# Kernel tuning notes

Measured on AMD Instinct MI355X. Metric: run time of the kernel, lower is better.

The kernel has to match this reference:

```python
import jax, jax.numpy as jnp
import numpy as np

B, T, H, NH, DH, R = 2, 2048, 1024, 16, 64, 256
ALPHA = 0.6


def setup_inputs() -> dict:
    key = jax.random.key(0)
    ks = jax.random.split(key, 28)
    f32 = jnp.float32

    def nrm(k, shape, s=0.02):
        return jax.random.normal(k, shape, dtype=f32) * s

    inp = {}
    inp['x'] = jax.random.normal(ks[0], (B, T, H), dtype=f32)
    # additive causal mask [1,1,T,T]: 0 on/below diagonal, -1e9 above
    causal = jnp.tril(jnp.ones((T, T), dtype=bool))
    inp['attention_mask'] = jnp.where(causal, 0.0, -1e9).astype(f32)[None, None]
    # low-rank SVD factors for q,k,v,o: Vh [H,R], S [R] (positive), U [H,R], b [H]
    i = 1
    for name in ('q', 'k', 'v', 'o'):
        inp['Vh_' + name] = nrm(ks[i], (H, R)); i += 1
        inp['S_' + name] = jax.random.uniform(ks[i], (R,), dtype=f32, minval=0.5, maxval=1.5); i += 1
        inp['U_' + name] = nrm(ks[i], (H, R)); i += 1
        inp['b_' + name] = jnp.zeros((H,), dtype=f32); i += 1
    # full-rank weights of the original (fallback) attention: y = x @ W + b (Conv1D style)
    for name in ('q', 'k', 'v', 'o'):
        inp['W_' + name] = nrm(ks[i], (H, H)); i += 1
        inp['bf_' + name] = jnp.zeros((H,), dtype=f32); i += 1
    return inp


def _split_heads(t):
    # [B,T,H] -> [B,nH,T,dH]
    Bs, Ts, _ = t.shape
    return t.reshape(Bs, Ts, NH, DH).transpose(0, 2, 1, 3)


def _attention(Q, K, V, mask):
    q, k, v = _split_heads(Q), _split_heads(K), _split_heads(V)
    scores = jnp.einsum('bhtd,bhsd->bhts', q, k) / (DH ** 0.5)
    scores = scores + mask
    w = jax.nn.softmax(scores, axis=-1)
    ctx = jnp.einsum('bhts,bhsd->bhtd', w, v)
    Bs = ctx.shape[0]
    return ctx.transpose(0, 2, 1, 3).reshape(Bs, -1, NH * DH)


def _lowrank(x, Vh, S, U, b):
    # ((x @ Vh) * S) @ U.T + b
    return ((x @ Vh) * S) @ U.T + b


def reference(x, attention_mask,
              Vh_q, S_q, U_q, b_q, Vh_k, S_k, U_k, b_k,
              Vh_v, S_v, U_v, b_v, Vh_o, S_o, U_o, b_o,
              W_q, bf_q, W_k, bf_k, W_v, bf_v, W_o, bf_o):
    # --- low-rank SVD path ---
    Q = _lowrank(x, Vh_q, S_q, U_q, b_q)
    K = _lowrank(x, Vh_k, S_k, U_k, b_k)
    V = _lowrank(x, Vh_v, S_v, U_v, b_v)
    ctx = _attention(Q, K, V, attention_mask)
    out = _lowrank(ctx, Vh_o, S_o, U_o, b_o)
    # --- fallback: original full-rank attention ---
    Qf = x @ W_q + bf_q
    Kf = x @ W_k + bf_k
    Vf = x @ W_v + bf_v
    ctxf = _attention(Qf, Kf, Vf, attention_mask)
    fallback_out = ctxf @ W_o + bf_o
    return ALPHA * out + (1.0 - ALPHA) * fallback_out
```

## Files before the change

kernel.cpp:

```cpp
#include <hip/hip_runtime.h>
#include <hip/hip_bf16.h>

typedef __bf16 bf16_t;
typedef __bf16 bf16x8 __attribute__((ext_vector_type(8)));
typedef float f32x4 __attribute__((ext_vector_type(4)));
typedef _Float16 f16_t;
typedef _Float16 f16x4 __attribute__((ext_vector_type(4)));

#define DEVI static __device__ __forceinline__

static constexpr int TN   = 2048;
static constexpr int Hn   = 1024;
static constexpr int Rn   = 256;
static constexpr int MTOK = 4096;
static constexpr int NCAT = 6144;

static constexpr float QSCALE = 0.125f;
static constexpr float SOFT_OFF = 0.2959399f;

template <typename T>
DEVI void gload16(const T* g, T* l) {
    __builtin_amdgcn_global_load_lds(
        (const __attribute__((address_space(1))) void*)g,
        (__attribute__((address_space(3))) void*)l, 16, 0, 0);
}

DEVI float loadf(const void* base, int idx, bool bfm) {
    if (bfm) {
        unsigned int u = ((const unsigned short*)base)[idx];
        u <<= 16;
        return __builtin_bit_cast(float, u);
    }
    return ((const float*)base)[idx];
}
DEVI bool detect_bf16(const void* mask) {
    return fabsf(((const float*)mask)[0]) > 1.0f;
}

struct PrepArgs {
    const void *x, *mask;
    const void *Vh[4], *S[4], *U[4];
    const void *bb[4], *bfb[4];
    bf16_t *Xb, *Abuf, *Bbuf;
    float *biascat, *biaso;
};

__global__ void k_prep(PrepArgs a) {
    const bool bfm = detect_bf16(a.mask);
    const int bid = blockIdx.x;
    if (bid < 4096) {
        int i = (bid * 256 + threadIdx.x) * 4;
#pragma unroll
        for (int j = 0; j < 4; ++j) a.Xb[i + j] = (bf16_t)loadf(a.x, i + j, bfm);
    } else if (bid < 8192) {
        int idx = (bid - 4096) * 256 + threadIdx.x;
        int proj = idx >> 18;
        int e = idx & 262143;
        int r = e & 255;
        float s = loadf(a.S[proj], r, bfm);
        if (proj == 0) s *= QSCALE;
        if (proj == 3) s *= 0.6f;
        a.Abuf[idx] = (bf16_t)(loadf(a.U[proj], e, bfm) * s);
        a.Bbuf[idx] = (bf16_t)loadf(a.Vh[proj], e, bfm);
    } else {
        int i = (bid - 8192) * 256 + threadIdx.x;
        if (i < 1024)      a.biascat[i] = QSCALE * loadf(a.bb[0], i, bfm);
        else if (i < 2048) a.biascat[i] = loadf(a.bb[1], i - 1024, bfm);
        else if (i < 3072) a.biascat[i] = loadf(a.bb[2], i - 2048, bfm);
        else if (i < 4096) a.biascat[i] = QSCALE * loadf(a.bfb[0], i - 3072, bfm);
        else if (i < 5120) a.biascat[i] = loadf(a.bfb[1], i - 4096, bfm);
        else if (i < 6144) a.biascat[i] = loadf(a.bfb[2], i - 5120, bfm);
        else {
            int j = i - 6144;
            a.biaso[j] = 0.6f * loadf(a.bb[3], j, bfm) + 0.4f * loadf(a.bfb[3], j, bfm);
        }
    }
}

struct TransP { const void* W[4]; bf16_t* dst[4]; int ldd[4]; float scale[4]; const void* mask; };

__global__ void k_transpose4(TransP tp) {
    const bool bfm = detect_bf16(tp.mask);
    const int z = blockIdx.z;
    const void* W = tp.W[z];
    bf16_t* dst = tp.dst[z];
    const int ldd = tp.ldd[z];
    const float scale = tp.scale[z];
    __shared__ float t[32][33];
    int bx = blockIdx.x * 32, by = blockIdx.y * 32;
    int tx = threadIdx.x, ty = threadIdx.y;
#pragma unroll
    for (int k = 0; k < 32; k += 8)
        t[ty + k][tx] = loadf(W, (by + ty + k) * Hn + bx + tx, bfm);
    __syncthreads();
#pragma unroll
    for (int k = 0; k < 32; k += 8)
        dst[(size_t)(bx + ty + k) * ldd + by + tx] = (bf16_t)(scale * t[tx][ty + k]);
}

template <int MI>
DEVI void gemm_stage(const bf16_t* __restrict__ A, int lda,
                     const bf16_t* __restrict__ B, int ldb,
                     int bm, int bn, int kb, bf16_t* Ad, bf16_t* Bd) {
    const int tid = threadIdx.x;
    constexpr int MT = MI * 32;
#pragma unroll
    for (int u = tid; u < MT * 4; u += 256)
        gload16(&A[(size_t)(bm + (u >> 2)) * lda + kb + (u & 3) * 8], &Ad[u * 8]);
#pragma unroll
    for (int u = tid; u < 512; u += 256)
        gload16(&B[(size_t)(bn + (u >> 2)) * ldb + kb + (u & 3) * 8], &Bd[u * 8]);
}

template <int MI>
DEVI void gemm_core_db(const bf16_t* __restrict__ A, int lda,
                       const bf16_t* __restrict__ B, int ldb, int K,
                       bf16_t* Ab0, bf16_t* Ab1, bf16_t* Bb0, bf16_t* Bb1,
                       int bm, int bn, f32x4 (&acc)[MI][4]) {
    const int lane = threadIdx.x & 63;
    const int w    = threadIdx.x >> 6;
    const int wr   = (w >> 1) * (MI * 16);
    const int wc   = (w & 1) * 64;
    const int fr   = lane & 15;
    const int quad = lane >> 4;

#pragma unroll
    for (int i = 0; i < MI; ++i)
#pragma unroll
        for (int j = 0; j < 4; ++j) acc[i][j] = {0.f, 0.f, 0.f, 0.f};

    gemm_stage<MI>(A, lda, B, ldb, bm, bn, 0, Ab0, Bb0);

    const int nk = K >> 5;
    for (int kb = 0; kb < nk; ++kb) {
        const bf16_t* Ac = (kb & 1) ? Ab1 : Ab0;
        const bf16_t* Bc = (kb & 1) ? Bb1 : Bb0;
        __syncthreads();
        if (kb + 1 < nk)
            gemm_stage<MI>(A, lda, B, ldb, bm, bn, (kb + 1) * 32,
                           (kb & 1) ? Ab0 : Ab1, (kb & 1) ? Bb0 : Bb1);
        bf16x8 af[MI], bfv[4];
#pragma unroll
        for (int i = 0; i < MI; ++i)
            af[i] = *(const bf16x8*)&Ac[(wr + i * 16 + fr) * 32 + quad * 8];
#pragma unroll
        for (int j = 0; j < 4; ++j)
            bfv[j] = *(const bf16x8*)&Bc[(wc + j * 16 + fr) * 32 + quad * 8];
#pragma unroll
        for (int i = 0; i < MI; ++i)
#pragma unroll
            for (int j = 0; j < 4; ++j)
                acc[i][j] = __builtin_amdgcn_mfma_f32_16x16x32_bf16(af[i], bfv[j], acc[i][j], 0, 0, 0);
    }
}

template <int MI, bool OUT_DUAL, bool WRITE_VT, int SWZ>
__global__ __launch_bounds__(256)
void k_gemm(const bf16_t* __restrict__ A, int lda,
            const bf16_t* __restrict__ B, int ldb,
            void* __restrict__ C, int ldc, int K,
            const float* __restrict__ bias, const void* __restrict__ mask,
            f16_t* __restrict__ Vt_g) {
    constexpr int MT = MI * 32;
    struct GB { bf16_t A0[MT * 32]; bf16_t A1[MT * 32]; bf16_t B0[4096]; bf16_t B1[4096]; };
    union SM { GB g; f16_t Ls[WRITE_VT ? 128 * 136 : 8]; };
    __shared__ __align__(16) SM sm;

    int bm, bn;
    if constexpr (SWZ == 1) {
        const int id = blockIdx.x, xcd = id & 7, idx = id >> 3;
        bn = (xcd * 6 + idx % 6) * 128;
        bm = (idx / 6) * MT;
    } else if constexpr (SWZ == 2) {
        const int id = blockIdx.x, xcd = id & 7, idx = id >> 3;
        bm = (xcd * 8 + (idx & 7)) * MT;
        bn = (idx >> 3) * 128;
    } else {
        bm = blockIdx.x * MT;
        bn = blockIdx.y * 128;
    }

    const int tid  = threadIdx.x;
    const int lane = tid & 63;
    const int w    = tid >> 6;
    const int wr   = (w >> 1) * (MI * 16);
    const int wc   = (w & 1) * 64;
    const int fr   = lane & 15;
    const int quad = lane >> 4;

    f32x4 acc[MI][4];
    gemm_core_db<MI>(A, lda, B, ldb, K, sm.g.A0, sm.g.A1, sm.g.B0, sm.g.B1, bm, bn, acc);

    if constexpr (WRITE_VT) {
        const bool isV = (bn >= 2048 && bn < 3072) || (bn >= 5120);
        if (isV) {
            const int pth = (bn >= 5120) ? 1 : 0;
            const int colrel = bn - (pth ? 5120 : 2048);
            const int bb = bm >> 11;
            const int R0 = (pth * 32 + bb * 16 + (colrel >> 6)) * 64;
            const int tloc = bm & 2047;
            __syncthreads();
#pragma unroll
            for (int i = 0; i < MI; ++i) {
                const int t0 = wr + i * 16 + quad * 4;
#pragma unroll
                for (int j = 0; j < 4; ++j) {
                    const int c = wc + j * 16 + fr;
                    const float bv = bias[bn + c];
#pragma unroll
                    for (int r = 0; r < 4; ++r)
                        sm.Ls[c * 136 + t0 + r] = (f16_t)(acc[i][j][r] + bv);
                }
            }
            __syncthreads();
            const int c = tid >> 1, seg = tid & 1;
            f16_t* dst = &Vt_g[(size_t)(R0 + c) * TN + tloc + seg * 64];
            const f16_t* src = &sm.Ls[c * 136 + seg * 64];
#pragma unroll
            for (int e = 0; e < 8; ++e)
                *(uint4*)&dst[e * 8] = *(const uint4*)&src[e * 8];
            return;
        }
    }

    bool bfm = false;
    if constexpr (OUT_DUAL) bfm = detect_bf16(mask);
#pragma unroll
    for (int i = 0; i < MI; ++i) {
        const int row0 = bm + wr + i * 16 + quad * 4;
#pragma unroll
        for (int j = 0; j < 4; ++j) {
            const int col = bn + wc + j * 16 + fr;
            const float bv = bias ? bias[col] : 0.f;
#pragma unroll
            for (int r = 0; r < 4; ++r) {
                float v = acc[i][j][r] + bv;
                size_t ci = (size_t)(row0 + r) * ldc + col;
                if constexpr (OUT_DUAL) {
                    if (bfm) ((unsigned short*)C)[ci] = __builtin_bit_cast(unsigned short, (bf16_t)v);
                    else     ((float*)C)[ci] = v;
                } else {
                    ((bf16_t*)C)[ci] = (bf16_t)v;
                }
            }
        }
    }
}

__global__ __launch_bounds__(256)
void k_gemm_small4(const bf16_t* __restrict__ Abuf, const bf16_t* __restrict__ Bbuf,
                   bf16_t* __restrict__ Wcat, bf16_t* __restrict__ WoT) {
    __shared__ __align__(16) bf16_t A0[64 * 32], A1[64 * 32], B0[4096], B1[4096];
    const int z = blockIdx.z;
    const bf16_t* A = Abuf + (size_t)z * Hn * Rn;
    const bf16_t* B = Bbuf + (size_t)z * Hn * Rn;
    bf16_t* C = (z < 3) ? (Wcat + (size_t)z * Hn * Hn) : WoT;
    const int ldc = (z < 3) ? Hn : 2048;

    const int bm = blockIdx.x * 64, bn = blockIdx.y * 128;
    f32x4 acc[2][4];
    gemm_core_db<2>(A, Rn, B, Rn, Rn, A0, A1, B0, B1, bm, bn, acc);

    const int lane = threadIdx.x & 63;
    const int w    = threadIdx.x >> 6;
    const int wr   = (w >> 1) * 32;
    const int wc   = (w & 1) * 64;
    const int fr   = lane & 15;
    const int quad = lane >> 4;
#pragma unroll
    for (int i = 0; i < 2; ++i)
#pragma unroll
        for (int j = 0; j < 4; ++j)
#pragma unroll
            for (int r = 0; r < 4; ++r)
                C[(size_t)(bm + wr + i * 16 + quad * 4 + r) * ldc + bn + wc + j * 16 + fr]
                    = (bf16_t)acc[i][j][r];
}

__global__ __launch_bounds__(256, 4)
void k_flash6(const bf16_t* __restrict__ Y, const f16_t* __restrict__ Vt_g,
              bf16_t* __restrict__ Ctx) {
    const int id   = blockIdx.x;
    const int inst = id & 63;
    const int qt2  = 15 - (id >> 6);
    const int p = inst >> 5, b = (inst >> 4) & 1, h = inst & 15;

    const int tid  = threadIdx.x;
    const int lane = tid & 63;
    const int w    = tid >> 6;
    const int fr   = lane & 15;
    const int quad = lane >> 4;

    const int rowbase = b * TN;
    const int qbase   = qt2 * 128;
    const int qcol = p * 3072 + h * 64;
    const int kcol = qcol + 1024;
    const int ccol = p * 1024 + h * 64;

    __shared__ __align__(16) bf16_t Kb[2][2][64 * 32];
    __shared__ __align__(16) f16_t  Vb[2][64 * 64];

    const int r64 = tid >> 2;
    const int c8  = (tid & 3) * 8;

    size_t vsrc[2];
#pragma unroll
    for (int t = 0; t < 2; ++t) {
        int pp = w * 128 + t * 64 + lane;
        int d  = pp >> 3;
        vsrc[t] = (size_t)(inst * 64 + d) * TN + ((((pp & 7) - d) & 7) * 8);
    }

    f16x4 ones;
#pragma unroll
    for (int j = 0; j < 4; ++j) ones[j] = (f16_t)1.0f;

    bf16x8 qf[2][2];
#pragma unroll
    for (int s = 0; s < 2; ++s) {
        const size_t qrow = (size_t)(rowbase + qbase + s * 64 + w * 16 + fr) * NCAT + qcol;
        qf[s][0] = *(const bf16x8*)&Y[qrow + quad * 8];
        qf[s][1] = *(const bf16x8*)&Y[qrow + 32 + quad * 8];
    }

    f32x4 o[2][4], lacc[2];
#pragma unroll
    for (int s = 0; s < 2; ++s) {
        lacc[s] = {0.f, 0.f, 0.f, 0.f};
#pragma unroll
        for (int db = 0; db < 4; ++db) o[s][db] = {0.f, 0.f, 0.f, 0.f};
    }

    const int t0 = (quad >> 1) + (fr & 7);
    const int h4 = (quad & 1) * 4;

    const int kmax = 2 * qt2 + 1;

    auto stage = [&](int kt, int bsel) {
        const bf16_t* ksrc = &Y[(size_t)(rowbase + kt * 64 + r64) * NCAT + kcol + c8];
        gload16(ksrc,      &Kb[bsel][0][tid * 8]);
        gload16(ksrc + 32, &Kb[bsel][1][tid * 8]);
#pragma unroll
        for (int t = 0; t < 2; ++t)
            gload16(&Vt_g[vsrc[t] + kt * 64], &Vb[bsel][(w * 128 + t * 64 + lane) * 8]);
    };

    stage(0, 0);

    for (int kt = 0; kt <= kmax; ++kt) {
        const int cur = kt & 1;
        __syncthreads();
        if (kt < kmax) stage(kt + 1, cur ^ 1);

#pragma unroll
        for (int s = 0; s < 2; ++s) {
            const int dk = 2 * qt2 + s;
            if (kt > dk) continue;

            f32x4 sacc[4];
#pragma unroll
            for (int nb = 0; nb < 4; ++nb) {
                bf16x8 kf0 = *(const bf16x8*)&Kb[cur][0][(nb * 16 + fr) * 32 + quad * 8];
                bf16x8 kf1 = *(const bf16x8*)&Kb[cur][1][(nb * 16 + fr) * 32 + quad * 8];
                f32x4 t4 = {0.f, 0.f, 0.f, 0.f};
                t4 = __builtin_amdgcn_mfma_f32_16x16x32_bf16(kf0, qf[s][0], t4, 0, 0, 0);
                t4 = __builtin_amdgcn_mfma_f32_16x16x32_bf16(kf1, qf[s][1], t4, 0, 0, 0);
                sacc[nb] = t4;
            }
            if (kt == dk) {
                const int kl = quad * 4;
                const int ql = w * 16 + fr;
#pragma unroll
                for (int nb = 0; nb < 4; ++nb)
#pragma unroll
                    for (int r = 0; r < 4; ++r)
                        if (nb * 16 + kl + r > ql) sacc[nb][r] = -1e30f;
            }

            f16x4 pf[4];
#pragma unroll
            for (int nb = 0; nb < 4; ++nb)
#pragma unroll
                for (int r = 0; r < 4; ++r)
                    pf[nb][r] = (f16_t)__expf(sacc[nb][r] - SOFT_OFF);

#pragma unroll
            for (int nb = 0; nb < 4; ++nb)
                lacc[s] = __builtin_amdgcn_mfma_f32_16x16x16f16(pf[nb], ones, lacc[s], 0, 0, 0);

#pragma unroll
            for (int db = 0; db < 4; ++db) {
                const int vbase = (db * 16 + fr) * 64 + h4;
#pragma unroll
                for (int nb = 0; nb < 4; ++nb) {
                    f16x4 vf = *(const f16x4*)&Vb[cur][vbase + (((nb * 2 + t0) & 7) * 8)];
                    o[s][db] = __builtin_amdgcn_mfma_f32_16x16x16f16(pf[nb], vf, o[s][db], 0, 0, 0);
                }
            }
        }
    }

#pragma unroll
    for (int s = 0; s < 2; ++s)
#pragma unroll
        for (int r = 0; r < 4; ++r) {
            const float inv = 1.0f / lacc[s][r];
            const size_t trow = (size_t)(rowbase + qbase + s * 64 + w * 16 + quad * 4 + r);
#pragma unroll
            for (int db = 0; db < 4; ++db)
                Ctx[trow * 2048 + ccol + db * 16 + fr] = (bf16_t)(o[s][db][r] * inv);
        }
}

extern "C" void kernel_launch(void* const* d_in, const int* in_sizes, int n_in,
                              void* d_out, int out_size, void* d_ws, size_t ws_size,
                              hipStream_t stream) {
    const void* x    = d_in[0];
    const void* mask = d_in[1];
    const void* Vh[4] = { d_in[2],  d_in[6],  d_in[10], d_in[14] };
    const void* Sp[4] = { d_in[3],  d_in[7],  d_in[11], d_in[15] };
    const void* Up[4] = { d_in[4],  d_in[8],  d_in[12], d_in[16] };
    const void* bb[4] = { d_in[5],  d_in[9],  d_in[13], d_in[17] };
    const void* Wp[4] = { d_in[18], d_in[20], d_in[22], d_in[24] };
    const void* bf[4] = { d_in[19], d_in[21], d_in[23], d_in[25] };

    char* ws = (char*)d_ws;
    size_t off = 0;
    auto alloc = [&](size_t bytes) -> void* {
        void* p = ws + off;
        off = (off + bytes + 255) & ~(size_t)255;
        return p;
    };
    bf16_t* Xb      = (bf16_t*)alloc((size_t)MTOK * Hn * 2);
    bf16_t* Wcat    = (bf16_t*)alloc((size_t)NCAT * Hn * 2);
    bf16_t* Yb      = (bf16_t*)alloc((size_t)MTOK * NCAT * 2);
    bf16_t* Ctx     = (bf16_t*)alloc((size_t)MTOK * 2048 * 2);
    bf16_t* WoT     = (bf16_t*)alloc((size_t)Hn * 2048 * 2);
    f16_t*  Vt_g    = (f16_t*)alloc((size_t)64 * 64 * TN * 2);
    bf16_t* Abuf    = (bf16_t*)alloc((size_t)4 * Hn * Rn * 2);
    bf16_t* Bbuf    = (bf16_t*)alloc((size_t)4 * Hn * Rn * 2);
    float*  biascat = (float*)alloc(NCAT * 4);
    float*  biaso   = (float*)alloc(Hn * 4);

    PrepArgs pa;
    pa.x = x; pa.mask = mask;
    for (int i = 0; i < 4; ++i) {
        pa.Vh[i] = Vh[i]; pa.S[i] = Sp[i]; pa.U[i] = Up[i];
        pa.bb[i] = bb[i]; pa.bfb[i] = bf[i];
    }
    pa.Xb = Xb; pa.Abuf = Abuf; pa.Bbuf = Bbuf; pa.biascat = biascat; pa.biaso = biaso;
    k_prep<<<8220, 256, 0, stream>>>(pa);

    TransP tp;
    for (int i = 0; i < 3; ++i) {
        tp.W[i] = Wp[i]; tp.dst[i] = Wcat + (size_t)(3 * Hn + i * Hn) * Hn;
        tp.ldd[i] = Hn; tp.scale[i] = (i == 0) ? QSCALE : 1.0f;
    }
    tp.W[3] = Wp[3]; tp.dst[3] = WoT + 1024; tp.ldd[3] = 2048; tp.scale[3] = 0.4f;
    tp.mask = mask;
    k_transpose4<<<dim3(32, 32, 4), dim3(32, 8), 0, stream>>>(tp);

    k_gemm_small4<<<dim3(16, 8, 4), 256, 0, stream>>>(Abuf, Bbuf, Wcat, WoT);

    k_gemm<4, false, true, 1><<<1536, 256, 0, stream>>>(
        Xb, Hn, Wcat, Hn, Yb, NCAT, Hn, biascat, nullptr, Vt_g);

    k_flash6<<<1024, 256, 0, stream>>>(Yb, Vt_g, Ctx);

    k_gemm<2, true, false, 2><<<512, 256, 0, stream>>>(
        Ctx, 2048, WoT, 2048, d_out, Hn, 2048, biaso, mask, nullptr);
}
```

Baseline: 325.0 us.

## Split-K the output projection GEMM and fold weight transpose into prep kernel

The final output GEMM (K=2048) is split into two K=1024 halves using larger 128-row tiles, each writing fp32 partials into the reused Yb buffer. A new combine kernel sums the partials, adds the bias and writes the output in the detected dtype. The separate weight-transpose launch is merged into the prep kernel as extra blocks to save a launch. The cost is an extra fp32 round trip of 2x4096x1024 partials plus one more kernel.

```diff
diff --git a/kernel.cpp b/kernel.cpp
--- a/kernel.cpp
+++ b/kernel.cpp
@@ -41,6 +41,8 @@
     const void *x, *mask;
     const void *Vh[4], *S[4], *U[4];
     const void *bb[4], *bfb[4];
+    const void *W[4];
+    bf16_t *Wdst[4]; int Wldd[4]; float Wscale[4];
     bf16_t *Xb, *Abuf, *Bbuf;
     float *biascat, *biaso;
 };
@@ -48,12 +50,14 @@
 __global__ void k_prep(PrepArgs a) {
     const bool bfm = detect_bf16(a.mask);
     const int bid = blockIdx.x;
+    const int tid = threadIdx.x;
+    __shared__ float t[32][33];
     if (bid < 4096) {
-        int i = (bid * 256 + threadIdx.x) * 4;
+        int i = (bid * 256 + tid) * 4;
 #pragma unroll
         for (int j = 0; j < 4; ++j) a.Xb[i + j] = (bf16_t)loadf(a.x, i + j, bfm);
     } else if (bid < 8192) {
-        int idx = (bid - 4096) * 256 + threadIdx.x;
+        int idx = (bid - 4096) * 256 + tid;
         int proj = idx >> 18;
         int e = idx & 262143;
         int r = e & 255;
@@ -62,8 +66,8 @@
         if (proj == 3) s *= 0.6f;
         a.Abuf[idx] = (bf16_t)(loadf(a.U[proj], e, bfm) * s);
         a.Bbuf[idx] = (bf16_t)loadf(a.Vh[proj], e, bfm);
-    } else {
-        int i = (bid - 8192) * 256 + threadIdx.x;
+    } else if (bid < 8220) {
+        int i = (bid - 8192) * 256 + tid;
         if (i < 1024)      a.biascat[i] = QSCALE * loadf(a.bb[0], i, bfm);
         else if (i < 2048) a.biascat[i] = loadf(a.bb[1], i - 1024, bfm);
         else if (i < 3072) a.biascat[i] = loadf(a.bb[2], i - 2048, bfm);
@@ -74,28 +78,24 @@
             int j = i - 6144;
             a.biaso[j] = 0.6f * loadf(a.bb[3], j, bfm) + 0.4f * loadf(a.bfb[3], j, bfm);
         }
-    }
-}
-
-struct TransP { const void* W[4]; bf16_t* dst[4]; int ldd[4]; float scale[4]; const void* mask; };
-
-__global__ void k_transpose4(TransP tp) {
-    const bool bfm = detect_bf16(tp.mask);
-    const int z = blockIdx.z;
-    const void* W = tp.W[z];
-    bf16_t* dst = tp.dst[z];
-    const int ldd = tp.ldd[z];
-    const float scale = tp.scale[z];
-    __shared__ float t[32][33];
-    int bx = blockIdx.x * 32, by = blockIdx.y * 32;
-    int tx = threadIdx.x, ty = threadIdx.y;
-#pragma unroll
-    for (int k = 0; k < 32; k += 8)
-        t[ty + k][tx] = loadf(W, (by + ty + k) * Hn + bx + tx, bfm);
-    __syncthreads();
-#pragma unroll
-    for (int k = 0; k < 32; k += 8)
-        dst[(size_t)(bx + ty + k) * ldd + by + tx] = (bf16_t)(scale * t[tx][ty + k]);
+    } else {
+        const int tb = bid - 8220;
+        const int z = tb >> 10;
+        const int t2 = tb & 1023;
+        const int bx = (t2 & 31) * 32, by = (t2 >> 5) * 32;
+        const int tx = tid & 31, ty = tid >> 5;
+        const void* W = a.W[z];
+        bf16_t* dst = a.Wdst[z];
+        const int ldd = a.Wldd[z];
+        const float scale = a.Wscale[z];
+#pragma unroll
+        for (int k = 0; k < 32; k += 8)
+            t[ty + k][tx] = loadf(W, (by + ty + k) * Hn + bx + tx, bfm);
+        __syncthreads();
+#pragma unroll
+        for (int k = 0; k < 32; k += 8)
+            dst[(size_t)(bx + ty + k) * ldd + by + tx] = (bf16_t)(scale * t[tx][ty + k]);
+    }
 }
 
 template <int MI>
@@ -154,13 +154,12 @@
     }
 }
 
-template <int MI, bool OUT_DUAL, bool WRITE_VT, int SWZ>
+template <int MI, int OMODE, bool WRITE_VT, int SWZ>
 __global__ __launch_bounds__(256)
 void k_gemm(const bf16_t* __restrict__ A, int lda,
             const bf16_t* __restrict__ B, int ldb,
             void* __restrict__ C, int ldc, int K,
-            const float* __restrict__ bias, const void* __restrict__ mask,
-            f16_t* __restrict__ Vt_g) {
+            const float* __restrict__ bias, f16_t* __restrict__ Vt_g) {
     constexpr int MT = MI * 32;
     struct GB { bf16_t A0[MT * 32]; bf16_t A1[MT * 32]; bf16_t B0[4096]; bf16_t B1[4096]; };
     union SM { GB g; f16_t Ls[WRITE_VT ? 128 * 136 : 8]; };
@@ -171,10 +170,15 @@
         const int id = blockIdx.x, xcd = id & 7, idx = id >> 3;
         bn = (xcd * 6 + idx % 6) * 128;
         bm = (idx / 6) * MT;
-    } else if constexpr (SWZ == 2) {
-        const int id = blockIdx.x, xcd = id & 7, idx = id >> 3;
-        bm = (xcd * 8 + (idx & 7)) * MT;
-        bn = (idx >> 3) * 128;
+    } else if constexpr (SWZ == 3) {
+        const int id = blockIdx.x;
+        const int ksel = id >> 8;
+        const int idx  = id & 255;
+        bn = (idx & 7) * 128;
+        bm = (idx >> 3) * MT;
+        A += ksel * 1024;
+        B += ksel * 1024;
+        C = (void*)((float*)C + (size_t)ksel * MTOK * 1024);
     } else {
         bm = blockIdx.x * MT;
         bn = blockIdx.y * 128;
@@ -223,27 +227,36 @@
         }
     }
 
-    bool bfm = false;
-    if constexpr (OUT_DUAL) bfm = detect_bf16(mask);
 #pragma unroll
     for (int i = 0; i < MI; ++i) {
         const int row0 = bm + wr + i * 16 + quad * 4;
 #pragma unroll
         for (int j = 0; j < 4; ++j) {
             const int col = bn + wc + j * 16 + fr;
-            const float bv = bias ? bias[col] : 0.f;
+            const float bv = (OMODE == 0 && bias) ? bias[col] : 0.f;
 #pragma unroll
             for (int r = 0; r < 4; ++r) {
                 float v = acc[i][j][r] + bv;
                 size_t ci = (size_t)(row0 + r) * ldc + col;
-                if constexpr (OUT_DUAL) {
-                    if (bfm) ((unsigned short*)C)[ci] = __builtin_bit_cast(unsigned short, (bf16_t)v);
-                    else     ((float*)C)[ci] = v;
-                } else {
-                    ((bf16_t*)C)[ci] = (bf16_t)v;
-                }
+                if constexpr (OMODE == 2) ((float*)C)[ci] = v;
+                else                      ((bf16_t*)C)[ci] = (bf16_t)v;
             }
         }
+    }
+}
+
+__global__ void k_combine(const float* __restrict__ P, const float* __restrict__ biaso,
+                          void* __restrict__ out, const void* __restrict__ mask) {
+    const bool bfm = detect_bf16(mask);
+    const int i = (blockIdx.x * 256 + threadIdx.x) * 4;
+    const f32x4 p0 = *(const f32x4*)&P[i];
+    const f32x4 p1 = *(const f32x4*)&P[i + MTOK * 1024];
+    const int col = i & 1023;
+#pragma unroll
+    for (int j = 0; j < 4; ++j) {
+        float v = p0[j] + p1[j] + biaso[col + j];
+        if (bfm) ((unsigned short*)out)[i + j] = __builtin_bit_cast(unsigned short, (bf16_t)v);
+        else     ((float*)out)[i + j] = v;
     }
 }
 
@@ -441,32 +454,32 @@
     bf16_t* Bbuf    = (bf16_t*)alloc((size_t)4 * Hn * Rn * 2);
     float*  biascat = (float*)alloc(NCAT * 4);
     float*  biaso   = (float*)alloc(Hn * 4);
+    float*  Psplit  = (float*)Yb;
 
     PrepArgs pa;
     pa.x = x; pa.mask = mask;
     for (int i = 0; i < 4; ++i) {
         pa.Vh[i] = Vh[i]; pa.S[i] = Sp[i]; pa.U[i] = Up[i];
         pa.bb[i] = bb[i]; pa.bfb[i] = bf[i];
-    }
+        pa.W[i] = Wp[i];
+    }
+    for (int i = 0; i < 3; ++i) {
+        pa.Wdst[i] = Wcat + (size_t)(3 * Hn + i * Hn) * Hn;
+        pa.Wldd[i] = Hn; pa.Wscale[i] = (i == 0) ? QSCALE : 1.0f;
+    }
+    pa.Wdst[3] = WoT + 1024; pa.Wldd[3] = 2048; pa.Wscale[3] = 0.4f;
     pa.Xb = Xb; pa.Abuf = Abuf; pa.Bbuf = Bbuf; pa.biascat = biascat; pa.biaso = biaso;
-    k_prep<<<8220, 256, 0, stream>>>(pa);
-
-    TransP tp;
-    for (int i = 0; i < 3; ++i) {
-        tp.W[i] = Wp[i]; tp.dst[i] = Wcat + (size_t)(3 * Hn + i * Hn) * Hn;
-        tp.ldd[i] = Hn; tp.scale[i] = (i == 0) ? QSCALE : 1.0f;
-    }
-    tp.W[3] = Wp[3]; tp.dst[3] = WoT + 1024; tp.ldd[3] = 2048; tp.scale[3] = 0.4f;
-    tp.mask = mask;
-    k_transpose4<<<dim3(32, 32, 4), dim3(32, 8), 0, stream>>>(tp);
+    k_prep<<<12316, 256, 0, stream>>>(pa);
 
     k_gemm_small4<<<dim3(16, 8, 4), 256, 0, stream>>>(Abuf, Bbuf, Wcat, WoT);
 
-    k_gemm<4, false, true, 1><<<1536, 256, 0, stream>>>(
-        Xb, Hn, Wcat, Hn, Yb, NCAT, Hn, biascat, nullptr, Vt_g);
+    k_gemm<4, 0, true, 1><<<1536, 256, 0, stream>>>(
+        Xb, Hn, Wcat, Hn, Yb, NCAT, Hn, biascat, Vt_g);
 
     k_flash6<<<1024, 256, 0, stream>>>(Yb, Vt_g, Ctx);
 
-    k_gemm<2, true, false, 2><<<512, 256, 0, stream>>>(
-        Ctx, 2048, WoT, 2048, d_out, Hn, 2048, biaso, mask, nullptr);
-}
+    k_gemm<4, 2, false, 3><<<512, 256, 0, stream>>>(
+        Ctx, 2048, WoT, 2048, Psplit, 1024, 1024, nullptr, nullptr);
+
+    k_combine<<<4096, 256, 0, stream>>>(Psplit, biaso, d_out, mask);
+}
```

Result: no change. 320.4 us (-1.4%).
